# Kernel tuning notes

Measured on AMD Instinct MI355X. Metric: run time of the kernel, lower is better.

Reference implementation:

```python
import jax, jax.numpy as jnp
import numpy as np

B, S, D, H = 2, 2048, 2048, 16
HD = D // H  # head_dim = 128
ROPE_THETA = 10000.0
NEG = -1e9


def _rotate_half(x):
    x1, x2 = jnp.split(x, 2, axis=-1)
    return jnp.concatenate([-x2, x1], axis=-1)


def setup_inputs() -> dict:
    key = jax.random.key(0)
    ks = jax.random.split(key, 6)
    scale = 1.0 / np.sqrt(D)
    hidden_states = jax.random.normal(ks[0], (B, S, D), dtype=jnp.float32)
    # additive causal mask: 0 on/below diagonal, large negative above
    causal = jnp.triu(jnp.full((S, S), NEG, dtype=jnp.float32), k=1)
    attention_mask = jnp.broadcast_to(causal[None, None], (B, 1, S, S))
    position_ids = jnp.broadcast_to(jnp.arange(S, dtype=jnp.int64)[None], (B, S))
    Wq = jax.random.normal(ks[1], (D, D), dtype=jnp.float32) * scale
    Wk = jax.random.normal(ks[2], (D, D), dtype=jnp.float32) * scale
    Wv = jax.random.normal(ks[3], (D, D), dtype=jnp.float32) * scale
    Wo = jax.random.normal(ks[4], (D, D), dtype=jnp.float32) * scale
    return dict(hidden_states=hidden_states, attention_mask=attention_mask,
                position_ids=position_ids, Wq=Wq, Wk=Wk, Wv=Wv, Wo=Wo)


def reference(hidden_states, attention_mask, position_ids, Wq, Wk, Wv, Wo):
    b, s, d = hidden_states.shape
    # projections (weights stored [in, out])
    q = (hidden_states @ Wq).reshape(b, s, H, HD).transpose(0, 2, 1, 3)  # bhsd
    k = (hidden_states @ Wk).reshape(b, s, H, HD).transpose(0, 2, 1, 3)
    v = (hidden_states @ Wv).reshape(b, s, H, HD).transpose(0, 2, 1, 3)
    # rotary embeddings
    inv_freq = 1.0 / (ROPE_THETA ** (jnp.arange(0, HD, 2, dtype=jnp.float32) / HD))
    freqs = position_ids.astype(jnp.float32)[..., None] * inv_freq  # [b, s, HD/2]
    emb = jnp.concatenate([freqs, freqs], axis=-1)
    cos = jnp.cos(emb)[:, None]  # [b, 1, s, HD]
    sin = jnp.sin(emb)[:, None]
    q = q * cos + _rotate_half(q) * sin
    k = k * cos + _rotate_half(k) * sin
    # attention
    scores = jnp.einsum('bhqd,bhkd->bhqk', q, k) / jnp.sqrt(jnp.float32(HD))
    scores = scores + attention_mask
    probs = jax.nn.softmax(scores.astype(jnp.float32), axis=-1).astype(q.dtype)
    out = jnp.einsum('bhqk,bhkd->bhqd', probs, v)
    out = out.transpose(0, 2, 1, 3).reshape(b, s, d)
    return out @ Wo
```

## Files before the change

### kernel.cpp

```cpp
#include <hip/hip_runtime.h>
#include <hip/hip_bf16.h>

#define Bv 2
#define Sv 2048
#define Dv 2048
#define Hv 16
#define HDv 128

typedef short bf16x8 __attribute__((ext_vector_type(8)));
typedef float f32x4 __attribute__((ext_vector_type(4)));

__device__ inline float b2f(unsigned short u) {
  union { unsigned int i; float f; } x; x.i = ((unsigned int)u) << 16; return x.f;
}
__device__ inline unsigned short f2b(float f) {
  union { float f; unsigned int u; } x; x.f = f;
  unsigned int r = (x.u + 0x7fffu + ((x.u >> 16) & 1u)) >> 16;
  return (unsigned short)r;
}

#define GLL16(gsrc, ldst)                                                      \
  __builtin_amdgcn_global_load_lds(                                            \
      (__attribute__((address_space(1))) void*)(gsrc),                         \
      (__attribute__((address_space(3))) void*)(ldst), 16, 0, 0)

__global__ __launch_bounds__(256) void f2b_kernel(const float4* __restrict__ in,
                                                  ushort4* __restrict__ out, int n4) {
  int i = blockIdx.x * 256 + threadIdx.x;
  if (i >= n4) return;
  float4 v = in[i];
  ushort4 r;
  r.x = f2b(v.x); r.y = f2b(v.y); r.z = f2b(v.z); r.w = f2b(v.w);
  out[i] = r;
}

__global__ void wtrans_kernel(const float* __restrict__ W, short* __restrict__ WT) {
  __shared__ float tile[32][33];
  int tx = threadIdx.x, ty = threadIdx.y;
  int c0 = blockIdx.x * 32, r0 = blockIdx.y * 32;
#pragma unroll
  for (int i = 0; i < 4; i++)
    tile[ty + i * 8][tx] = W[(long)(r0 + ty + i * 8) * Dv + c0 + tx];
  __syncthreads();
#pragma unroll
  for (int i = 0; i < 4; i++)
    WT[(long)(c0 + ty + i * 8) * Dv + r0 + tx] = (short)f2b(tile[tx][ty + i * 8]);
}

__global__ __launch_bounds__(256) void rope_table_kernel(float* __restrict__ tab) {
  int i = blockIdx.x * 256 + threadIdx.x;
  int s = i >> 6, d = i & 63;
  float inv = powf(10000.f, -(float)d * (1.f / 64.f));
  float ang = (float)s * inv;
  tab[s * 128 + d] = cosf(ang);
  tab[s * 128 + 64 + d] = sinf(ang);
}

__global__ __launch_bounds__(256) void rope_kernel(short* __restrict__ T,
                                                   const float* __restrict__ tab) {
  int tid = blockIdx.x * 256 + threadIdx.x;
  int r = tid >> 3, j = tid & 7;
  int s = r & (Sv - 1);
  short* p = T + (long)r * HDv + j * 8;
  bf16x8 a = *(const bf16x8*)p;
  bf16x8 bb = *(const bf16x8*)(p + 64);
  const float* tc = tab + s * 128 + j * 8;
  float4 c0 = *(const float4*)tc, c1 = *(const float4*)(tc + 4);
  float4 s0 = *(const float4*)(tc + 64), s1 = *(const float4*)(tc + 68);
  float cs[8] = {c0.x, c0.y, c0.z, c0.w, c1.x, c1.y, c1.z, c1.w};
  float sn[8] = {s0.x, s0.y, s0.z, s0.w, s1.x, s1.y, s1.z, s1.w};
  bf16x8 na, nb;
#pragma unroll
  for (int e = 0; e < 8; e++) {
    float x1 = b2f((unsigned short)a[e]);
    float x2 = b2f((unsigned short)bb[e]);
    na[e] = (short)f2b(x1 * cs[e] - x2 * sn[e]);
    nb[e] = (short)f2b(x2 * cs[e] + x1 * sn[e]);
  }
  *(bf16x8*)p = na;
  *(bf16x8*)(p + 64) = nb;
}

template <int MODE>
__global__ __launch_bounds__(256) void gemm_kernel(const short* __restrict__ A,
                                                   const short* __restrict__ Bt,
                                                   void* __restrict__ Cout,
                                                   int M, int N, int K) {
  __shared__ __align__(16) short As[128 * 32];
  __shared__ __align__(16) short Bs[128 * 32];
  const int t = threadIdx.x, w = t >> 6, l = t & 63;
  const int m0 = blockIdx.y * 128, n0 = blockIdx.x * 128;
  const int wr = w >> 1, wc = w & 1;
  f32x4 acc[4][4] = {};
  const short* ag = A + (long)(m0 + (t >> 2)) * K + (t & 3) * 8;
  const short* bg = Bt + (long)(n0 + (t >> 2)) * K + (t & 3) * 8;
  short* asw = As + (w * 16) * 32;
  short* bsw = Bs + (w * 16) * 32;
  const int aoff = (wr * 64 + (l & 15)) * 32 + (l >> 4) * 8;
  const int boff = (wc * 64 + (l & 15)) * 32 + (l >> 4) * 8;
  for (int k0 = 0; k0 < K; k0 += 32) {
    GLL16(ag + k0, asw);
    GLL16(ag + (long)64 * K + k0, asw + 64 * 32);
    GLL16(bg + k0, bsw);
    GLL16(bg + (long)64 * K + k0, bsw + 64 * 32);
    __syncthreads();
    bf16x8 af[4], bf[4];
#pragma unroll
    for (int i = 0; i < 4; i++) af[i] = *(const bf16x8*)(As + aoff + i * 16 * 32);
#pragma unroll
    for (int i = 0; i < 4; i++) bf[i] = *(const bf16x8*)(Bs + boff + i * 16 * 32);
#pragma unroll
    for (int i = 0; i < 4; i++)
#pragma unroll
      for (int j = 0; j < 4; j++)
        acc[i][j] = __builtin_amdgcn_mfma_f32_16x16x32_bf16(af[i], bf[j], acc[i][j], 0, 0, 0);
    __syncthreads();
  }
  const int fr = l >> 4;
#pragma unroll
  for (int mi = 0; mi < 4; mi++) {
#pragma unroll
    for (int ni = 0; ni < 4; ni++) {
      f32x4 v = acc[mi][ni];
      int col = n0 + wc * 64 + ni * 16 + (l & 15);
      int mbase = m0 + wr * 64 + mi * 16 + fr * 4;
      if (MODE == 0) {
        short* qkv = (short*)Cout;
        int which = col >> 11, hn = col & 2047;
        int h = hn >> 7, d = hn & 127;
#pragma unroll
        for (int j = 0; j < 4; j++) {
          int m = mbase + j;
          int b = m >> 11, s = m & 2047;
          qkv[(long)which * 8388608 + (((long)(b * Hv + h)) * Sv + s) * HDv + d] =
              (short)f2b(v[j]);
        }
      } else {
        float* C = (float*)Cout;
#pragma unroll
        for (int j = 0; j < 4; j++) C[(long)(mbase + j) * N + col] = v[j];
      }
    }
  }
}

__global__ __launch_bounds__(256) void attn_kernel(const short* __restrict__ Q,
                                                   const short* __restrict__ Kk,
                                                   const short* __restrict__ V,
                                                   short* __restrict__ O) {
  __shared__ __align__(16) short k_s[64 * 128];
  __shared__ __align__(16) short vt_s[128 * 72];
  __shared__ __align__(16) short p_s[4 * 16 * 72];
  const int t = threadIdx.x, w = t >> 6, l = t & 63;
  const int g = l >> 4, a = l & 15;
  const int bh = blockIdx.y, qb = blockIdx.x;
  const int q0w = qb * 64 + w * 16;
  const short* Qb = Q + (long)bh * Sv * HDv;
  const short* Kb = Kk + (long)bh * Sv * HDv;
  const short* Vb = V + (long)bh * Sv * HDv;

  bf16x8 qf[4];
#pragma unroll
  for (int kk = 0; kk < 4; kk++)
    qf[kk] = *(const bf16x8*)(Qb + (long)(q0w + a) * HDv + kk * 32 + g * 8);

  f32x4 acc_o[8] = {};
  float m_run[4] = {-1e30f, -1e30f, -1e30f, -1e30f};
  float l_run[4] = {0.f, 0.f, 0.f, 0.f};
  const float scale = 0.08838834764831845f;

  for (int kb = 0; kb <= qb; ++kb) {
    const int kv0 = kb * 64;
    __syncthreads();
#pragma unroll
    for (int j = 0; j < 4; j++) {
      int grow = kv0 + j * 16 + w * 4 + g;
      const short* src = Kb + (long)grow * HDv + ((a * 8) ^ ((grow & 15) << 3));
      GLL16(src, k_s + j * 2048 + w * 512);
    }
    {
      const short* vrow = Vb + (long)(kv0 + l) * HDv + w * 32;
      bf16x8 vv[4];
#pragma unroll
      for (int j = 0; j < 4; j++) vv[j] = *(const bf16x8*)(vrow + j * 8);
#pragma unroll
      for (int i = 0; i < 32; i++) {
        int row = w * 32 + i;
        vt_s[row * 72 + (l ^ ((row & 7) << 3))] = vv[i >> 3][i & 7];
      }
    }
    __syncthreads();
    f32x4 sacc[4] = {};
#pragma unroll
    for (int ksb = 0; ksb < 4; ksb++) {
      int row = ksb * 16 + a;
#pragma unroll
      for (int kk = 0; kk < 4; kk++) {
        bf16x8 kf = *(const bf16x8*)(k_s + row * 128 + ((kk * 32 + g * 8) ^ ((row & 15) << 3)));
        sacc[ksb] = __builtin_amdgcn_mfma_f32_16x16x32_bf16(qf[kk], kf, sacc[ksb], 0, 0, 0);
      }
    }
    float s[4][4];
    const bool domask = (kb == qb);
#pragma unroll
    for (int ksb = 0; ksb < 4; ksb++)
#pragma unroll
      for (int r = 0; r < 4; r++) {
        float v = sacc[ksb][r] * scale;
        if (domask) {
          int key = kv0 + ksb * 16 + a, qq = q0w + g * 4 + r;
          v = (key <= qq) ? v : -1e30f;
        }
        s[ksb][r] = v;
      }
    float mnew[4], alpha[4];
#pragma unroll
    for (int r = 0; r < 4; r++) {
      float m = fmaxf(fmaxf(s[0][r], s[1][r]), fmaxf(s[2][r], s[3][r]));
      m = fmaxf(m, __shfl_xor(m, 1));
      m = fmaxf(m, __shfl_xor(m, 2));
      m = fmaxf(m, __shfl_xor(m, 4));
      m = fmaxf(m, __shfl_xor(m, 8));
      mnew[r] = fmaxf(m_run[r], m);
      alpha[r] = __expf(m_run[r] - mnew[r]);
      m_run[r] = mnew[r];
    }
    float rs[4] = {0.f, 0.f, 0.f, 0.f};
#pragma unroll
    for (int ksb = 0; ksb < 4; ksb++)
#pragma unroll
      for (int r = 0; r < 4; r++) {
        float p = __expf(s[ksb][r] - mnew[r]);
        s[ksb][r] = p;
        rs[r] += p;
      }
#pragma unroll
    for (int r = 0; r < 4; r++) {
      float x = rs[r];
      x += __shfl_xor(x, 1);
      x += __shfl_xor(x, 2);
      x += __shfl_xor(x, 4);
      x += __shfl_xor(x, 8);
      l_run[r] = l_run[r] * alpha[r] + x;
    }
#pragma unroll
    for (int ksb = 0; ksb < 4; ksb++)
#pragma unroll
      for (int r = 0; r < 4; r++) {
        int q_loc = g * 4 + r;
        p_s[w * 1152 + q_loc * 72 + ((ksb * 16 + a) ^ ((q_loc & 7) << 3))] =
            (short)f2b(s[ksb][r]);
      }
#pragma unroll
    for (int d = 0; d < 8; d++)
#pragma unroll
      for (int r = 0; r < 4; r++) acc_o[d][r] *= alpha[r];
    bf16x8 pa[2];
#pragma unroll
    for (int kc = 0; kc < 2; kc++)
      pa[kc] = *(const bf16x8*)(p_s + w * 1152 + a * 72 + ((kc * 32 + g * 8) ^ ((a & 7) << 3)));
#pragma unroll
    for (int d = 0; d < 8; d++) {
      int row = d * 16 + a;
#pragma unroll
      for (int kc = 0; kc < 2; kc++) {
        bf16x8 vf = *(const bf16x8*)(vt_s + row * 72 + ((kc * 32 + g * 8) ^ ((row & 7) << 3)));
        acc_o[d] = __builtin_amdgcn_mfma_f32_16x16x32_bf16(pa[kc], vf, acc_o[d], 0, 0, 0);
      }
    }
  }
  const int b = bh >> 4, h = bh & 15;
#pragma unroll
  for (int r = 0; r < 4; r++) {
    float inv = 1.f / l_run[r];
    int q = q0w + g * 4 + r;
    short* orow = O + ((long)(b * Sv + q)) * Dv + h * HDv + a;
#pragma unroll
    for (int d = 0; d < 8; d++) orow[d * 16] = (short)f2b(acc_o[d][r] * inv);
  }
}

extern "C" void kernel_launch(void* const* d_in, const int* in_sizes, int n_in,
                              void* d_out, int out_size, void* d_ws, size_t ws_size,
                              hipStream_t stream) {
  const float* X = (const float*)d_in[0];
  const float* Wq = (const float*)d_in[3];
  const float* Wk = (const float*)d_in[4];
  const float* Wv = (const float*)d_in[5];
  const float* Wo = (const float*)d_in[6];
  float* out = (float*)d_out;

  short* XB = (short*)d_ws;
  short* WQKVT = XB + 8388608;
  short* WOT = WQKVT + 12582912;
  short* QKV = WOT + 4194304;
  float* TAB = (float*)(QKV + 25165824);
  short* AO = XB;

  f2b_kernel<<<8192, 256, 0, stream>>>((const float4*)X, (ushort4*)XB, 2097152);
  dim3 wtb(32, 8), wtg(64, 64);
  wtrans_kernel<<<wtg, wtb, 0, stream>>>(Wq, WQKVT);
  wtrans_kernel<<<wtg, wtb, 0, stream>>>(Wk, WQKVT + 4194304);
  wtrans_kernel<<<wtg, wtb, 0, stream>>>(Wv, WQKVT + 8388608);
  wtrans_kernel<<<wtg, wtb, 0, stream>>>(Wo, WOT);
  rope_table_kernel<<<512, 256, 0, stream>>>(TAB);
  gemm_kernel<0><<<dim3(48, 32), 256, 0, stream>>>(XB, WQKVT, QKV, 4096, 6144, 2048);
  rope_kernel<<<2048, 256, 0, stream>>>(QKV, TAB);
  rope_kernel<<<2048, 256, 0, stream>>>(QKV + 8388608, TAB);
  attn_kernel<<<dim3(32, 32), 256, 0, stream>>>(QKV, QKV + 8388608, QKV + 16777216, AO);
  gemm_kernel<1><<<dim3(16, 32), 256, 0, stream>>>(AO, WOT, out, 4096, 2048, 2048);
}
```

Baseline: 585.0 us.

## Pre-transpose V globally and stream it into LDS with async loads

```diff
diff --git a/kernel.cpp b/kernel.cpp
--- a/kernel.cpp
+++ b/kernel.cpp
@@ -45,6 +45,21 @@
 #pragma unroll
   for (int i = 0; i < 4; i++)
     WT[(long)(c0 + ty + i * 8) * Dv + r0 + tx] = (short)f2b(tile[tx][ty + i * 8]);
+}
+
+__global__ void vtrans_kernel(const short* __restrict__ V, short* __restrict__ VT) {
+  __shared__ short tile[32][33];
+  int tx = threadIdx.x, ty = threadIdx.y;
+  int k0 = blockIdx.x * 32, d0 = blockIdx.y * 32, bh = blockIdx.z;
+  const short* src = V + (long)bh * Sv * HDv;
+  short* dst = VT + (long)bh * HDv * Sv;
+#pragma unroll
+  for (int i = 0; i < 4; i++)
+    tile[ty + i * 8][tx] = src[(long)(k0 + ty + i * 8) * HDv + d0 + tx];
+  __syncthreads();
+#pragma unroll
+  for (int i = 0; i < 4; i++)
+    dst[(long)(d0 + ty + i * 8) * Sv + k0 + tx] = tile[tx][ty + i * 8];
 }
 
 __global__ __launch_bounds__(256) void rope_table_kernel(float* __restrict__ tab) {
@@ -146,18 +161,19 @@
 
 __global__ __launch_bounds__(256) void attn_kernel(const short* __restrict__ Q,
                                                    const short* __restrict__ Kk,
-                                                   const short* __restrict__ V,
+                                                   const short* __restrict__ VT,
                                                    short* __restrict__ O) {
   __shared__ __align__(16) short k_s[64 * 128];
-  __shared__ __align__(16) short vt_s[128 * 72];
-  __shared__ __align__(16) short p_s[4 * 16 * 72];
+  __shared__ __align__(16) short vt_s[64 * 128];
+  __shared__ __align__(16) short p_s[4 * 16 * 64];
   const int t = threadIdx.x, w = t >> 6, l = t & 63;
   const int g = l >> 4, a = l & 15;
-  const int bh = blockIdx.y, qb = blockIdx.x;
+  const int bh = blockIdx.y;
+  const int qb = (gridDim.x - 1) - blockIdx.x;
   const int q0w = qb * 64 + w * 16;
   const short* Qb = Q + (long)bh * Sv * HDv;
   const short* Kb = Kk + (long)bh * Sv * HDv;
-  const short* Vb = V + (long)bh * Sv * HDv;
+  const short* VTb = VT + (long)bh * HDv * Sv;
 
   bf16x8 qf[4];
 #pragma unroll
@@ -169,25 +185,23 @@
   float l_run[4] = {0.f, 0.f, 0.f, 0.f};
   const float scale = 0.08838834764831845f;
 
+  const int rr = l >> 4, sub = l & 15;
+
   for (int kb = 0; kb <= qb; ++kb) {
     const int kv0 = kb * 64;
     __syncthreads();
 #pragma unroll
     for (int j = 0; j < 4; j++) {
-      int grow = kv0 + j * 16 + w * 4 + g;
-      const short* src = Kb + (long)grow * HDv + ((a * 8) ^ ((grow & 15) << 3));
-      GLL16(src, k_s + j * 2048 + w * 512);
-    }
-    {
-      const short* vrow = Vb + (long)(kv0 + l) * HDv + w * 32;
-      bf16x8 vv[4];
-#pragma unroll
-      for (int j = 0; j < 4; j++) vv[j] = *(const bf16x8*)(vrow + j * 8);
-#pragma unroll
-      for (int i = 0; i < 32; i++) {
-        int row = w * 32 + i;
-        vt_s[row * 72 + (l ^ ((row & 7) << 3))] = vv[i >> 3][i & 7];
-      }
+      int row = j * 16 + w * 4 + rr;
+      int c0 = (sub * 8) ^ ((row & 15) << 3);
+      GLL16(Kb + (long)(kv0 + row) * HDv + c0, k_s + (j * 16 + w * 4) * 128);
+    }
+#pragma unroll
+    for (int j = 0; j < 4; j++) {
+      int row = w * 16 + j * 4 + rr;
+      int c0 = (sub * 8) ^ ((row & 15) << 3);
+      int d = row + (c0 & 64);
+      GLL16(VTb + (long)d * Sv + kv0 + (c0 & 63), vt_s + (w * 16 + j * 4) * 128);
     }
     __syncthreads();
     f32x4 sacc[4] = {};
@@ -248,7 +262,7 @@
 #pragma unroll
       for (int r = 0; r < 4; r++) {
         int q_loc = g * 4 + r;
-        p_s[w * 1152 + q_loc * 72 + ((ksb * 16 + a) ^ ((q_loc & 7) << 3))] =
+        p_s[w * 1024 + q_loc * 64 + ((ksb * 16 + a) ^ ((q_loc & 7) << 3))] =
             (short)f2b(s[ksb][r]);
       }
 #pragma unroll
@@ -258,14 +272,16 @@
     bf16x8 pa[2];
 #pragma unroll
     for (int kc = 0; kc < 2; kc++)
-      pa[kc] = *(const bf16x8*)(p_s + w * 1152 + a * 72 + ((kc * 32 + g * 8) ^ ((a & 7) << 3)));
-#pragma unroll
-    for (int d = 0; d < 8; d++) {
-      int row = d * 16 + a;
+      pa[kc] = *(const bf16x8*)(p_s + w * 1024 + a * 64 + ((kc * 32 + g * 8) ^ ((a & 7) << 3)));
+#pragma unroll
+    for (int dblk = 0; dblk < 8; dblk++) {
+      int row = (dblk & 3) * 16 + a;
+      int half = (dblk >> 2) * 64;
 #pragma unroll
       for (int kc = 0; kc < 2; kc++) {
-        bf16x8 vf = *(const bf16x8*)(vt_s + row * 72 + ((kc * 32 + g * 8) ^ ((row & 7) << 3)));
-        acc_o[d] = __builtin_amdgcn_mfma_f32_16x16x32_bf16(pa[kc], vf, acc_o[d], 0, 0, 0);
+        bf16x8 vf = *(const bf16x8*)(vt_s + row * 128 +
+                                     ((half + kc * 32 + g * 8) ^ ((row & 15) << 3)));
+        acc_o[dblk] = __builtin_amdgcn_mfma_f32_16x16x32_bf16(pa[kc], vf, acc_o[dblk], 0, 0, 0);
       }
     }
   }
@@ -296,6 +312,7 @@
   short* QKV = WOT + 4194304;
   float* TAB = (float*)(QKV + 25165824);
   short* AO = XB;
+  short* VTG = WQKVT;
 
   f2b_kernel<<<8192, 256, 0, stream>>>((const float4*)X, (ushort4*)XB, 2097152);
   dim3 wtb(32, 8), wtg(64, 64);
@@ -305,8 +322,8 @@
   wtrans_kernel<<<wtg, wtb, 0, stream>>>(Wo, WOT);
   rope_table_kernel<<<512, 256, 0, stream>>>(TAB);
   gemm_kernel<0><<<dim3(48, 32), 256, 0, stream>>>(XB, WQKVT, QKV, 4096, 6144, 2048);
-  rope_kernel<<<2048, 256, 0, stream>>>(QKV, TAB);
-  rope_kernel<<<2048, 256, 0, stream>>>(QKV + 8388608, TAB);
-  attn_kernel<<<dim3(32, 32), 256, 0, stream>>>(QKV, QKV + 8388608, QKV + 16777216, AO);
+  rope_kernel<<<4096, 256, 0, stream>>>(QKV, TAB);
+  vtrans_kernel<<<dim3(64, 4, 32), wtb, 0, stream>>>(QKV + 16777216, VTG);
+  attn_kernel<<<dim3(32, 32), 256, 0, stream>>>(QKV, QKV + 8388608, VTG, AO);
   gemm_kernel<1><<<dim3(16, 32), 256, 0, stream>>>(AO, WOT, out, 4096, 2048, 2048);
 }
```

After: 682.7 us. 1.17x slower.
